# Optimization experiments

Measured on AMD Instinct MI355X. Metric: run time of the kernel, lower is better.

The kernel has to match this reference:

```python
import jax, jax.numpy as jnp
import numpy as np

B, S, H, NH = 2, 2048, 2048, 16
HD = H // NH
SCALE = 1.0 / np.sqrt(HD).astype(np.float32)


def setup_inputs() -> dict:
    key = jax.random.key(0)
    ks = jax.random.split(key, 11)
    std = 1.0 / np.sqrt(H)
    inp = {
        'query': jax.random.normal(ks[0], (B, S, H), dtype=jnp.float32),
        'key': jax.random.normal(ks[1], (B, S, H), dtype=jnp.float32),
        'value': jax.random.normal(ks[2], (B, S, H), dtype=jnp.float32),
        'Wq': jax.random.normal(ks[3], (H, H), dtype=jnp.float32) * std,
        'bq': jax.random.normal(ks[4], (H,), dtype=jnp.float32) * std,
        'Wk': jax.random.normal(ks[5], (H, H), dtype=jnp.float32) * std,
        'bk': jax.random.normal(ks[6], (H,), dtype=jnp.float32) * std,
        'Wv': jax.random.normal(ks[7], (H, H), dtype=jnp.float32) * std,
        'bv': jax.random.normal(ks[8], (H,), dtype=jnp.float32) * std,
        'Wo': jax.random.normal(ks[9], (H, H), dtype=jnp.float32) * std,
        'bo': jax.random.normal(ks[10], (H,), dtype=jnp.float32) * std,
    }
    return inp


def reference(query, key, value, Wq, bq, Wk, bk, Wv, bv, Wo, bo):
    # Linear projections (torch Linear: x @ W.T + b)
    q = query @ Wq.T + bq
    k = key @ Wk.T + bk
    v = value @ Wv.T + bv
    # [B, NH, S, HD]
    q = q.reshape(B, S, NH, HD).transpose(0, 2, 1, 3)
    k = k.reshape(B, S, NH, HD).transpose(0, 2, 1, 3)
    v = v.reshape(B, S, NH, HD).transpose(0, 2, 1, 3)
    scores = jnp.einsum('bhqd,bhkd->bhqk', q, k) * SCALE
    attn = jax.nn.softmax(scores, axis=-1)  # dropout p=0 (eval)
    ctx = jnp.einsum('bhqk,bhkd->bhqd', attn, v)
    ctx = ctx.transpose(0, 2, 1, 3).reshape(B, S, H)
    out = ctx @ Wo.T + bo
    return out
```

## Files before the change

kernel.cpp:

```cpp
#include <hip/hip_runtime.h>


typedef __bf16 bf16_t;
typedef __bf16 bf16x8 __attribute__((ext_vector_type(8)));
typedef float  f32x4  __attribute__((ext_vector_type(4)));

#define DEVI __device__ __forceinline__

DEVI void async_copy16(const void* gsrc, void* ldst) {
  __builtin_amdgcn_global_load_lds(
      (const __attribute__((address_space(1))) unsigned int*)gsrc,
      (__attribute__((address_space(3))) unsigned int*)ldst, 16, 0, 0);
}

constexpr int Bc = 2, Sc = 2048, Hc = 2048, NHc = 16, HDc = 128;
constexpr float SCALE_F = 0.088388347648318447f;

__global__ void cast_f32_to_bf16(const float* __restrict__ in,
                                 bf16_t* __restrict__ out, int n) {
  int i = (blockIdx.x * 256 + threadIdx.x) * 8;
  if (i >= n) return;
  float4 f0 = *(const float4*)(in + i);
  float4 f1 = *(const float4*)(in + i + 4);
  union { bf16_t h[8]; uint4 u; } o;
  o.h[0] = (bf16_t)f0.x; o.h[1] = (bf16_t)f0.y;
  o.h[2] = (bf16_t)f0.z; o.h[3] = (bf16_t)f0.w;
  o.h[4] = (bf16_t)f1.x; o.h[5] = (bf16_t)f1.y;
  o.h[6] = (bf16_t)f1.z; o.h[7] = (bf16_t)f1.w;
  *(uint4*)(out + i) = o.u;
}

template <int M, int N, int K, int OUT_MODE>
__global__ __launch_bounds__(256, 2) void gemm_bt(const bf16_t* __restrict__ A,
                                                  const bf16_t* __restrict__ Bw,
                                                  const float* __restrict__ bias,
                                                  void* __restrict__ Cout) {
  constexpr int BM = 128, BN = 128, BK = 64;
  __shared__ __align__(16) bf16_t As[BM * BK];
  __shared__ __align__(16) bf16_t Bs[BN * BK];
  const int tid = threadIdx.x;
  const int lane = tid & 63;
  const int wave = tid >> 6;
  const int bm = blockIdx.x & (M / BM - 1);
  const int bn = blockIdx.x / (M / BM);
  const int wm = wave >> 1, wn = wave & 1;
  const int quad = lane >> 4, l15 = lane & 15;

  int s_r[4], s_c[4];
#pragma unroll
  for (int i = 0; i < 4; ++i) {
    int seg = wave * 4 + i;
    int r = seg * 8 + (lane >> 3);
    s_r[i] = r;
    s_c[i] = (lane & 7) ^ (r & 7);
  }
  const bf16_t* Abase = A + (size_t)bm * BM * K;
  const bf16_t* Bbase = Bw + (size_t)bn * BN * K;

  f32x4 zero4 = {0.f, 0.f, 0.f, 0.f};
  f32x4 acc[4][4];
#pragma unroll
  for (int i = 0; i < 4; ++i)
#pragma unroll
    for (int j = 0; j < 4; ++j) acc[i][j] = zero4;

  int arow[4], brow[4];
#pragma unroll
  for (int t = 0; t < 4; ++t) {
    arow[t] = wm * 64 + t * 16 + l15;
    brow[t] = wn * 64 + t * 16 + l15;
  }

  for (int kt = 0; kt < K / BK; ++kt) {
    const int k0 = kt * BK;
#pragma unroll
    for (int i = 0; i < 4; ++i) {
      int seg = wave * 4 + i;
      async_copy16(Abase + (size_t)s_r[i] * K + k0 + s_c[i] * 8, As + seg * 512);
      async_copy16(Bbase + (size_t)s_r[i] * K + k0 + s_c[i] * 8, Bs + seg * 512);
    }
    __syncthreads();
#pragma unroll
    for (int ks = 0; ks < 2; ++ks) {
      bf16x8 af[4], bfv[4];
#pragma unroll
      for (int mt = 0; mt < 4; ++mt)
        af[mt] = *(const bf16x8*)(As + arow[mt] * 64 +
                                  (((ks * 4 + quad) ^ (arow[mt] & 7)) * 8));
#pragma unroll
      for (int nt = 0; nt < 4; ++nt)
        bfv[nt] = *(const bf16x8*)(Bs + brow[nt] * 64 +
                                   (((ks * 4 + quad) ^ (brow[nt] & 7)) * 8));
#pragma unroll
      for (int mt = 0; mt < 4; ++mt)
#pragma unroll
        for (int nt = 0; nt < 4; ++nt)
          acc[mt][nt] = __builtin_amdgcn_mfma_f32_16x16x32_bf16(
              af[mt], bfv[nt], acc[mt][nt], 0, 0, 0);
    }
    __syncthreads();
  }

  float bv[4];
#pragma unroll
  for (int nt = 0; nt < 4; ++nt) bv[nt] = bias[bn * BN + brow[nt]];

#pragma unroll
  for (int mt = 0; mt < 4; ++mt) {
    const int rbase = bm * BM + wm * 64 + mt * 16 + quad * 4;
#pragma unroll
    for (int nt = 0; nt < 4; ++nt) {
      const int col = bn * BN + brow[nt];
      if constexpr (OUT_MODE == 0) {
        bf16_t* C = (bf16_t*)Cout;
#pragma unroll
        for (int r = 0; r < 4; ++r)
          C[(size_t)(rbase + r) * N + col] = (bf16_t)(acc[mt][nt][r] + bv[nt]);
      } else if constexpr (OUT_MODE == 2) {
        float* C = (float*)Cout;
#pragma unroll
        for (int r = 0; r < 4; ++r)
          C[(size_t)(rbase + r) * N + col] = acc[mt][nt][r] + bv[nt];
      } else {
        bf16_t* C = (bf16_t*)Cout;
        const int bb = rbase >> 11;
        const int s0 = rbase & (Sc - 1);
        const int h = col >> 7, d = col & (HDc - 1);
        union { bf16_t h4[4]; uint2 u; } o;
#pragma unroll
        for (int r = 0; r < 4; ++r) o.h4[r] = (bf16_t)(acc[mt][nt][r] + bv[nt]);
        *(uint2*)(C + (((size_t)(bb * NHc + h) * HDc + d) * Sc + s0)) = o.u;
      }
    }
  }
}

__global__ __launch_bounds__(256, 1) void flash_attn(const bf16_t* __restrict__ Q,
                                                     const bf16_t* __restrict__ Kg,
                                                     const bf16_t* __restrict__ Vt,
                                                     bf16_t* __restrict__ ctx) {
  extern __shared__ char smem[];
  bf16_t* Ks = (bf16_t*)smem;
  bf16_t* Vs = (bf16_t*)(smem + 32768);
  float* Ps = (float*)(smem + 65536);

  const int tid = threadIdx.x, lane = tid & 63, wave = tid >> 6;
  const int quad = lane >> 4, l15 = lane & 15;
  const int bid = blockIdx.x;
  const int qt = bid & 15, h = (bid >> 4) & 15, b = bid >> 8;

  float* Pw = Ps + wave * (32 * 132);

  bf16x8 qf[2][4];
#pragma unroll
  for (int mt = 0; mt < 2; ++mt) {
    int grow = b * Sc + qt * 128 + wave * 32 + mt * 16 + l15;
    const bf16_t* qp = Q + (size_t)grow * Hc + h * HDc;
#pragma unroll
    for (int kc = 0; kc < 4; ++kc) qf[mt][kc] = *(const bf16x8*)(qp + kc * 32 + quad * 8);
  }

  f32x4 zero4 = {0.f, 0.f, 0.f, 0.f};
  f32x4 o[2][8];
#pragma unroll
  for (int mt = 0; mt < 2; ++mt)
#pragma unroll
    for (int dt = 0; dt < 8; ++dt) o[mt][dt] = zero4;
  float mrow[2][4], lrow[2][4];
#pragma unroll
  for (int mt = 0; mt < 2; ++mt)
#pragma unroll
    for (int r = 0; r < 4; ++r) { mrow[mt][r] = -1e30f; lrow[mt][r] = 0.f; }

  int st_r[8], st_c[8];
#pragma unroll
  for (int i = 0; i < 8; ++i) {
    int seg = wave * 8 + i;
    st_r[i] = seg * 4 + (lane >> 4);
    st_c[i] = (lane & 15) ^ (st_r[i] & 7);
  }
  const bf16_t* Kbase = Kg + (size_t)b * Sc * Hc + h * HDc;
  const bf16_t* Vbase = Vt + (size_t)(b * NHc + h) * HDc * Sc;

  for (int kb = 0; kb < 16; ++kb) {
#pragma unroll
    for (int i = 0; i < 8; ++i) {
      int seg = wave * 8 + i;
      async_copy16(Kbase + (size_t)(kb * 128 + st_r[i]) * Hc + st_c[i] * 8, Ks + seg * 512);
      async_copy16(Vbase + (size_t)st_r[i] * Sc + kb * 128 + st_c[i] * 8, Vs + seg * 512);
    }
    __syncthreads();

    f32x4 sf[2][8];
#pragma unroll
    for (int mt = 0; mt < 2; ++mt)
#pragma unroll
      for (int nt = 0; nt < 8; ++nt) sf[mt][nt] = zero4;
#pragma unroll
    for (int kc = 0; kc < 4; ++kc)
#pragma unroll
      for (int nt = 0; nt < 8; ++nt) {
        int kr = nt * 16 + l15;
        bf16x8 kf = *(const bf16x8*)(Ks + kr * 128 + (((kc * 4 + quad) ^ (kr & 7)) * 8));
        sf[0][nt] = __builtin_amdgcn_mfma_f32_16x16x32_bf16(qf[0][kc], kf, sf[0][nt], 0, 0, 0);
        sf[1][nt] = __builtin_amdgcn_mfma_f32_16x16x32_bf16(qf[1][kc], kf, sf[1][nt], 0, 0, 0);
      }

#pragma unroll
    for (int mt = 0; mt < 2; ++mt)
#pragma unroll
      for (int r = 0; r < 4; ++r) {
        float mx = sf[mt][0][r];
#pragma unroll
        for (int nt = 1; nt < 8; ++nt) mx = fmaxf(mx, sf[mt][nt][r]);
#pragma unroll
        for (int off = 1; off < 16; off <<= 1) mx = fmaxf(mx, __shfl_xor(mx, off));
        float mnew = fmaxf(mrow[mt][r], mx);
        float alpha = __expf((mrow[mt][r] - mnew) * SCALE_F);
        float msc = mnew * SCALE_F;
        float rs = 0.f;
#pragma unroll
        for (int nt = 0; nt < 8; ++nt) {
          float p = __expf(sf[mt][nt][r] * SCALE_F - msc);
          sf[mt][nt][r] = p;
          rs += p;
        }
#pragma unroll
        for (int off = 1; off < 16; off <<= 1) rs += __shfl_xor(rs, off);
        lrow[mt][r] = lrow[mt][r] * alpha + rs;
        mrow[mt][r] = mnew;
#pragma unroll
        for (int dt = 0; dt < 8; ++dt) o[mt][dt][r] *= alpha;
      }

#pragma unroll
    for (int mt = 0; mt < 2; ++mt)
#pragma unroll
      for (int nt = 0; nt < 8; ++nt)
#pragma unroll
        for (int r = 0; r < 4; ++r)
          Pw[(mt * 16 + quad * 4 + r) * 132 + nt * 16 + l15] = sf[mt][nt][r];

    bf16x8 pf[2][4];
#pragma unroll
    for (int mt = 0; mt < 2; ++mt) {
      const float* pr = Pw + (mt * 16 + l15) * 132;
#pragma unroll
      for (int kc = 0; kc < 4; ++kc) {
        f32x4 x0 = *(const f32x4*)(pr + kc * 32 + quad * 8);
        f32x4 x1 = *(const f32x4*)(pr + kc * 32 + quad * 8 + 4);
        bf16x8 t;
        t[0] = (bf16_t)x0[0]; t[1] = (bf16_t)x0[1]; t[2] = (bf16_t)x0[2]; t[3] = (bf16_t)x0[3];
        t[4] = (bf16_t)x1[0]; t[5] = (bf16_t)x1[1]; t[6] = (bf16_t)x1[2]; t[7] = (bf16_t)x1[3];
        pf[mt][kc] = t;
      }
    }

#pragma unroll
    for (int kc = 0; kc < 4; ++kc)
#pragma unroll
      for (int dt = 0; dt < 8; ++dt) {
        int vr = dt * 16 + l15;
        bf16x8 vf = *(const bf16x8*)(Vs + vr * 128 + (((kc * 4 + quad) ^ (vr & 7)) * 8));
        o[0][dt] = __builtin_amdgcn_mfma_f32_16x16x32_bf16(pf[0][kc], vf, o[0][dt], 0, 0, 0);
        o[1][dt] = __builtin_amdgcn_mfma_f32_16x16x32_bf16(pf[1][kc], vf, o[1][dt], 0, 0, 0);
      }
    __syncthreads();
  }

#pragma unroll
  for (int mt = 0; mt < 2; ++mt) {
    float rinv[4];
#pragma unroll
    for (int r = 0; r < 4; ++r) rinv[r] = 1.f / lrow[mt][r];
#pragma unroll
    for (int dt = 0; dt < 8; ++dt)
#pragma unroll
      for (int r = 0; r < 4; ++r)
        Pw[(mt * 16 + quad * 4 + r) * 132 + dt * 16 + l15] = o[mt][dt][r] * rinv[r];
  }
#pragma unroll
  for (int r = 0; r < 32; ++r) {
    float2 v = *(const float2*)(Pw + r * 132 + lane * 2);
    union { bf16_t h[2]; unsigned u; } pk;
    pk.h[0] = (bf16_t)v.x; pk.h[1] = (bf16_t)v.y;
    int grow = b * Sc + qt * 128 + wave * 32 + r;
    *(unsigned*)(ctx + (size_t)grow * Hc + h * HDc + lane * 2) = pk.u;
  }
}

extern "C" void kernel_launch(void* const* d_in, const int* in_sizes, int n_in,
                              void* d_out, int out_size, void* d_ws, size_t ws_size,
                              hipStream_t stream) {
  const float* query = (const float*)d_in[0];
  const float* key_i = (const float*)d_in[1];
  const float* value = (const float*)d_in[2];
  const float* Wq = (const float*)d_in[3];
  const float* bq = (const float*)d_in[4];
  const float* Wk = (const float*)d_in[5];
  const float* bk = (const float*)d_in[6];
  const float* Wv = (const float*)d_in[7];
  const float* bv = (const float*)d_in[8];
  const float* Wo = (const float*)d_in[9];
  const float* bo = (const float*)d_in[10];

  const size_t XE = (size_t)Bc * Sc * Hc;
  const size_t WE = (size_t)Hc * Hc;
  const size_t need = 6 * XE * 2 + 4 * WE * 2;
  if (ws_size < need) return;

  char* ws = (char*)d_ws;
  size_t off = 0;
  auto alloc = [&](size_t bytes) {
    char* p = ws + off;
    off += (bytes + 255) & ~(size_t)255;
    return p;
  };
  bf16_t* Xq = (bf16_t*)alloc(XE * 2);
  bf16_t* Xk = (bf16_t*)alloc(XE * 2);
  bf16_t* Xv = (bf16_t*)alloc(XE * 2);
  bf16_t* Wqb = (bf16_t*)alloc(WE * 2);
  bf16_t* Wkb = (bf16_t*)alloc(WE * 2);
  bf16_t* Wvb = (bf16_t*)alloc(WE * 2);
  bf16_t* Wob = (bf16_t*)alloc(WE * 2);
  bf16_t* qb = (bf16_t*)alloc(XE * 2);
  bf16_t* kb = (bf16_t*)alloc(XE * 2);
  bf16_t* vtb = (bf16_t*)alloc(XE * 2);
  bf16_t* ctxb = Xq;

  cast_f32_to_bf16<<<(int)(XE / 2048), 256, 0, stream>>>(query, Xq, (int)XE);
  cast_f32_to_bf16<<<(int)(XE / 2048), 256, 0, stream>>>(key_i, Xk, (int)XE);
  cast_f32_to_bf16<<<(int)(XE / 2048), 256, 0, stream>>>(value, Xv, (int)XE);
  cast_f32_to_bf16<<<(int)(WE / 2048), 256, 0, stream>>>(Wq, Wqb, (int)WE);
  cast_f32_to_bf16<<<(int)(WE / 2048), 256, 0, stream>>>(Wk, Wkb, (int)WE);
  cast_f32_to_bf16<<<(int)(WE / 2048), 256, 0, stream>>>(Wv, Wvb, (int)WE);
  cast_f32_to_bf16<<<(int)(WE / 2048), 256, 0, stream>>>(Wo, Wob, (int)WE);

  gemm_bt<4096, 2048, 2048, 0><<<512, 256, 0, stream>>>(Xq, Wqb, bq, qb);
  gemm_bt<4096, 2048, 2048, 0><<<512, 256, 0, stream>>>(Xk, Wkb, bk, kb);
  gemm_bt<4096, 2048, 2048, 1><<<512, 256, 0, stream>>>(Xv, Wvb, bv, vtb);

  hipFuncSetAttribute((const void*)flash_attn,
                      hipFuncAttributeMaxDynamicSharedMemorySize, 133120);
  flash_attn<<<512, 256, 133120, stream>>>(qb, kb, vtb, ctxb);

  gemm_bt<4096, 2048, 2048, 2><<<512, 256, 0, stream>>>(ctxb, Wob, bo, (float*)d_out);
}
```

Measured before the change: 510.7 us.

## Batch cast launches, fold softmax scale into Q, store P in bf16 LDS

Merges the seven cast launches into two grid-batched kernels to cut launch overhead. Folds the softmax scale into the Q projection epilogue so the attention inner loop skips the per-element scale multiplies. Stores the P tile and output staging in LDS as bf16 instead of fp32, halving LDS traffic and footprint (133 KB down to 100 KB) and removing the conversion on readback. Rounding Q to bf16 after scaling changes numerics slightly.

```diff
diff --git a/kernel.cpp b/kernel.cpp
--- a/kernel.cpp
+++ b/kernel.cpp
@@ -15,11 +15,10 @@
 
 constexpr int Bc = 2, Sc = 2048, Hc = 2048, NHc = 16, HDc = 128;
 constexpr float SCALE_F = 0.088388347648318447f;
-
-__global__ void cast_f32_to_bf16(const float* __restrict__ in,
-                                 bf16_t* __restrict__ out, int n) {
+constexpr int PSTR = 136;
+
+DEVI void cast_body(const float* __restrict__ in, bf16_t* __restrict__ out) {
   int i = (blockIdx.x * 256 + threadIdx.x) * 8;
-  if (i >= n) return;
   float4 f0 = *(const float4*)(in + i);
   float4 f1 = *(const float4*)(in + i + 4);
   union { bf16_t h[8]; uint4 u; } o;
@@ -30,11 +29,31 @@
   *(uint4*)(out + i) = o.u;
 }
 
+__global__ void cast3(const float* __restrict__ a, const float* __restrict__ b,
+                      const float* __restrict__ c, bf16_t* __restrict__ oa,
+                      bf16_t* __restrict__ ob, bf16_t* __restrict__ oc) {
+  const float* src = blockIdx.y == 0 ? a : blockIdx.y == 1 ? b : c;
+  bf16_t* dst = blockIdx.y == 0 ? oa : blockIdx.y == 1 ? ob : oc;
+  cast_body(src, dst);
+}
+
+__global__ void cast4(const float* __restrict__ a, const float* __restrict__ b,
+                      const float* __restrict__ c, const float* __restrict__ d,
+                      bf16_t* __restrict__ oa, bf16_t* __restrict__ ob,
+                      bf16_t* __restrict__ oc, bf16_t* __restrict__ od) {
+  const float* src = blockIdx.y == 0 ? a : blockIdx.y == 1 ? b
+                   : blockIdx.y == 2 ? c : d;
+  bf16_t* dst = blockIdx.y == 0 ? oa : blockIdx.y == 1 ? ob
+              : blockIdx.y == 2 ? oc : od;
+  cast_body(src, dst);
+}
+
 template <int M, int N, int K, int OUT_MODE>
 __global__ __launch_bounds__(256, 2) void gemm_bt(const bf16_t* __restrict__ A,
                                                   const bf16_t* __restrict__ Bw,
                                                   const float* __restrict__ bias,
-                                                  void* __restrict__ Cout) {
+                                                  void* __restrict__ Cout,
+                                                  float scale) {
   constexpr int BM = 128, BN = 128, BK = 64;
   __shared__ __align__(16) bf16_t As[BM * BK];
   __shared__ __align__(16) bf16_t Bs[BN * BK];
@@ -115,7 +134,7 @@
         bf16_t* C = (bf16_t*)Cout;
 #pragma unroll
         for (int r = 0; r < 4; ++r)
-          C[(size_t)(rbase + r) * N + col] = (bf16_t)(acc[mt][nt][r] + bv[nt]);
+          C[(size_t)(rbase + r) * N + col] = (bf16_t)((acc[mt][nt][r] + bv[nt]) * scale);
       } else if constexpr (OUT_MODE == 2) {
         float* C = (float*)Cout;
 #pragma unroll
@@ -142,14 +161,14 @@
   extern __shared__ char smem[];
   bf16_t* Ks = (bf16_t*)smem;
   bf16_t* Vs = (bf16_t*)(smem + 32768);
-  float* Ps = (float*)(smem + 65536);
+  bf16_t* Ps = (bf16_t*)(smem + 65536);
 
   const int tid = threadIdx.x, lane = tid & 63, wave = tid >> 6;
   const int quad = lane >> 4, l15 = lane & 15;
   const int bid = blockIdx.x;
   const int qt = bid & 15, h = (bid >> 4) & 15, b = bid >> 8;
 
-  float* Pw = Ps + wave * (32 * 132);
+  bf16_t* Pw = Ps + wave * (32 * PSTR);
 
   bf16x8 qf[2][4];
 #pragma unroll
@@ -216,12 +235,11 @@
 #pragma unroll
         for (int off = 1; off < 16; off <<= 1) mx = fmaxf(mx, __shfl_xor(mx, off));
         float mnew = fmaxf(mrow[mt][r], mx);
-        float alpha = __expf((mrow[mt][r] - mnew) * SCALE_F);
-        float msc = mnew * SCALE_F;
+        float alpha = __expf(mrow[mt][r] - mnew);
         float rs = 0.f;
 #pragma unroll
         for (int nt = 0; nt < 8; ++nt) {
-          float p = __expf(sf[mt][nt][r] * SCALE_F - msc);
+          float p = __expf(sf[mt][nt][r] - mnew);
           sf[mt][nt][r] = p;
           rs += p;
         }
@@ -239,21 +257,15 @@
       for (int nt = 0; nt < 8; ++nt)
 #pragma unroll
         for (int r = 0; r < 4; ++r)
-          Pw[(mt * 16 + quad * 4 + r) * 132 + nt * 16 + l15] = sf[mt][nt][r];
+          Pw[(mt * 16 + quad * 4 + r) * PSTR + nt * 16 + l15] = (bf16_t)sf[mt][nt][r];
 
     bf16x8 pf[2][4];
 #pragma unroll
     for (int mt = 0; mt < 2; ++mt) {
-      const float* pr = Pw + (mt * 16 + l15) * 132;
-#pragma unroll
-      for (int kc = 0; kc < 4; ++kc) {
-        f32x4 x0 = *(const f32x4*)(pr + kc * 32 + quad * 8);
-        f32x4 x1 = *(const f32x4*)(pr + kc * 32 + quad * 8 + 4);
-        bf16x8 t;
-        t[0] = (bf16_t)x0[0]; t[1] = (bf16_t)x0[1]; t[2] = (bf16_t)x0[2]; t[3] = (bf16_t)x0[3];
-        t[4] = (bf16_t)x1[0]; t[5] = (bf16_t)x1[1]; t[6] = (bf16_t)x1[2]; t[7] = (bf16_t)x1[3];
-        pf[mt][kc] = t;
-      }
+      const bf16_t* pr = Pw + (mt * 16 + l15) * PSTR;
+#pragma unroll
+      for (int kc = 0; kc < 4; ++kc)
+        pf[mt][kc] = *(const bf16x8*)(pr + kc * 32 + quad * 8);
     }
 
 #pragma unroll
@@ -277,15 +289,13 @@
     for (int dt = 0; dt < 8; ++dt)
 #pragma unroll
       for (int r = 0; r < 4; ++r)
-        Pw[(mt * 16 + quad * 4 + r) * 132 + dt * 16 + l15] = o[mt][dt][r] * rinv[r];
+        Pw[(mt * 16 + quad * 4 + r) * PSTR + dt * 16 + l15] = (bf16_t)(o[mt][dt][r] * rinv[r]);
   }
 #pragma unroll
   for (int r = 0; r < 32; ++r) {
-    float2 v = *(const float2*)(Pw + r * 132 + lane * 2);
-    union { bf16_t h[2]; unsigned u; } pk;
-    pk.h[0] = (bf16_t)v.x; pk.h[1] = (bf16_t)v.y;
+    unsigned v = *(const unsigned*)(Pw + r * PSTR + lane * 2);
     int grow = b * Sc + qt * 128 + wave * 32 + r;
-    *(unsigned*)(ctx + (size_t)grow * Hc + h * HDc + lane * 2) = pk.u;
+    *(unsigned*)(ctx + (size_t)grow * Hc + h * HDc + lane * 2) = v;
   }
 }
 
@@ -328,21 +338,16 @@
   bf16_t* vtb = (bf16_t*)alloc(XE * 2);
   bf16_t* ctxb = Xq;
 
-  cast_f32_to_bf16<<<(int)(XE / 2048), 256, 0, stream>>>(query, Xq, (int)XE);
-  cast_f32_to_bf16<<<(int)(XE / 2048), 256, 0, stream>>>(key_i, Xk, (int)XE);
-  cast_f32_to_bf16<<<(int)(XE / 2048), 256, 0, stream>>>(value, Xv, (int)XE);
-  cast_f32_to_bf16<<<(int)(WE / 2048), 256, 0, stream>>>(Wq, Wqb, (int)WE);
-  cast_f32_to_bf16<<<(int)(WE / 2048), 256, 0, stream>>>(Wk, Wkb, (int)WE);
-  cast_f32_to_bf16<<<(int)(WE / 2048), 256, 0, stream>>>(Wv, Wvb, (int)WE);
-  cast_f32_to_bf16<<<(int)(WE / 2048), 256, 0, stream>>>(Wo, Wob, (int)WE);
-
-  gemm_bt<4096, 2048, 2048, 0><<<512, 256, 0, stream>>>(Xq, Wqb, bq, qb);
-  gemm_bt<4096, 2048, 2048, 0><<<512, 256, 0, stream>>>(Xk, Wkb, bk, kb);
-  gemm_bt<4096, 2048, 2048, 1><<<512, 256, 0, stream>>>(Xv, Wvb, bv, vtb);
+  cast3<<<dim3((unsigned)(XE / 2048), 3), 256, 0, stream>>>(query, key_i, value, Xq, Xk, Xv);
+  cast4<<<dim3((unsigned)(WE / 2048), 4), 256, 0, stream>>>(Wq, Wk, Wv, Wo, Wqb, Wkb, Wvb, Wob);
+
+  gemm_bt<4096, 2048, 2048, 0><<<512, 256, 0, stream>>>(Xq, Wqb, bq, qb, SCALE_F);
+  gemm_bt<4096, 2048, 2048, 0><<<512, 256, 0, stream>>>(Xk, Wkb, bk, kb, 1.0f);
+  gemm_bt<4096, 2048, 2048, 1><<<512, 256, 0, stream>>>(Xv, Wvb, bv, vtb, 1.0f);
 
   hipFuncSetAttribute((const void*)flash_attn,
-                      hipFuncAttributeMaxDynamicSharedMemorySize, 133120);
-  flash_attn<<<512, 256, 133120, stream>>>(qb, kb, vtb, ctxb);
-
-  gemm_bt<4096, 2048, 2048, 2><<<512, 256, 0, stream>>>(ctxb, Wob, bo, (float*)d_out);
-}
+                      hipFuncAttributeMaxDynamicSharedMemorySize, 100352);
+  flash_attn<<<512, 256, 100352, stream>>>(qb, kb, vtb, ctxb);
+
+  gemm_bt<4096, 2048, 2048, 2><<<512, 256, 0, stream>>>(ctxb, Wob, bo, (float*)d_out, 1.0f);
+}
```

After: 502.3 us. Within noise of the previous version (-1.6%).
